# Kernel tuning notes

Measured on AMD Instinct MI355X. Metric: run time of the kernel, lower is better.

The kernel has to match this reference:

```python
import jax, jax.numpy as jnp
import numpy as np

RANK = 16
ALPHA = 16.0
SCALING = ALPHA / RANK
N_ADAPTERS = 8
IN_F = 4096
OUT_F = 4096
BATCH = 4
SEQ = 2048


def setup_inputs() -> dict:
    key = jax.random.key(0)
    kx, ka, kb, ki = jax.random.split(key, 4)
    x = jax.random.normal(kx, (BATCH, SEQ, IN_F), dtype=jnp.float32)
    # A init: randn * 0.02 (as in module). B is zeros in the module; use small
    # random values here so the baseline output/grads are non-trivial.
    A = jax.random.normal(ka, (N_ADAPTERS, OUT_F, RANK), dtype=jnp.float32) * 0.02
    B = jax.random.normal(kb, (N_ADAPTERS, RANK, IN_F), dtype=jnp.float32) * 0.02
    adapter_ids = jax.random.randint(ki, (BATCH,), 0, N_ADAPTERS, dtype=jnp.int32)
    return {"x": x, "A": A, "B": B, "adapter_ids": adapter_ids}


def reference(x, A, B, adapter_ids):
    # Original: Bx = einsum('bni,ari->bnar', x, B); res = einsum('bnar,aor->bnao', Bx, A)
    # then res[arange(b), :, adapter_ids] * scaling.
    # Equivalent (gather-then-batched-GEMM): select each batch element's adapter
    # first, avoiding the O(n_adapters) dense intermediate. Same math.
    B_sel = B[adapter_ids]            # [b, r, in]
    A_sel = A[adapter_ids]            # [b, out, r]
    Bx = jnp.einsum('bni,bri->bnr', x, B_sel)   # [b, n, r]
    out = jnp.einsum('bnr,bor->bno', Bx, A_sel)  # [b, n, out]
    return out * SCALING
```

## Files before the change

### kernel.cpp

```cpp
#include <hip/hip_runtime.h>
#include <hip/hip_bf16.h>

#define RANK   16
#define IN_F   4096
#define OUT_F  4096
#define NBATCH 4
#define SEQLEN 2048
#define NROWS  (NBATCH * SEQLEN)

typedef __bf16 bf16x8   __attribute__((ext_vector_type(8)));
typedef float  floatx4  __attribute__((ext_vector_type(4)));
typedef float  floatx16 __attribute__((ext_vector_type(16)));

static __device__ __forceinline__ bf16x8 load_cvt8(const float* __restrict__ p) {
    floatx4 a = *reinterpret_cast<const floatx4*>(p);
    floatx4 b = *reinterpret_cast<const floatx4*>(p + 4);
    bf16x8 r;
    r[0] = (__bf16)a[0]; r[1] = (__bf16)a[1]; r[2] = (__bf16)a[2]; r[3] = (__bf16)a[3];
    r[4] = (__bf16)b[0]; r[5] = (__bf16)b[1]; r[6] = (__bf16)b[2]; r[7] = (__bf16)b[3];
    return r;
}

__global__ __launch_bounds__(256) void
lora_bx_kernel(const float* __restrict__ x, const float* __restrict__ Bw,
               const int* __restrict__ ids, __bf16* __restrict__ bx)
{
    const int tile = blockIdx.x;
    const int row0 = tile * 16;
    const int adapter = ids[row0 / SEQLEN];
    const int wave = threadIdx.x >> 6;
    const int lane = threadIdx.x & 63;
    const int m    = lane & 15;
    const int quad = lane >> 4;

    const float* xp = x + (size_t)(row0 + m) * IN_F + quad * 8 + wave * 1024;
    const float* bp = Bw + (size_t)adapter * (RANK * IN_F)
                         + (size_t)m * IN_F + quad * 8 + wave * 1024;

    floatx4 acc = {0.f, 0.f, 0.f, 0.f};
#pragma unroll 8
    for (int s = 0; s < 32; ++s) {
        bf16x8 af = load_cvt8(xp + s * 32);
        bf16x8 bf = load_cvt8(bp + s * 32);
        acc = __builtin_amdgcn_mfma_f32_16x16x32_bf16(af, bf, acc, 0, 0, 0);
    }

    __shared__ float red[4][256];
#pragma unroll
    for (int j = 0; j < 4; ++j)
        red[wave][(quad * 4 + j) * 16 + m] = acc[j];
    __syncthreads();

    const int t = threadIdx.x;
    float s = (red[0][t] + red[1][t]) + (red[2][t] + red[3][t]);
    bx[tile * 256 + t] = (__bf16)s;
}

__global__ __launch_bounds__(256) void
lora_out_kernel(const __bf16* __restrict__ bx, const float* __restrict__ Aw,
                const int* __restrict__ ids, float* __restrict__ out)
{
    const int rt    = blockIdx.x >> 2;
    const int chunk = blockIdx.x & 3;
    const int row0  = rt * 32;
    const int adapter = ids[row0 / SEQLEN];
    const int wave = threadIdx.x >> 6;
    const int lane = threadIdx.x & 63;
    const int n    = lane & 31;
    const int half = lane >> 5;

    const bf16x8 a_bx = *reinterpret_cast<const bf16x8*>(
        bx + rt * 512 + n * 16 + half * 8);

    const float* ap = Aw + (size_t)adapter * (OUT_F * RANK) + half * 8;
    const int colbase = chunk * 1024 + wave * 256;

#pragma unroll
    for (int tcol = 0; tcol < 8; ++tcol) {
        const int col0 = colbase + tcol * 32;
        bf16x8 bfrag = load_cvt8(ap + (size_t)(col0 + n) * RANK);
        floatx16 c;
#pragma unroll
        for (int i = 0; i < 16; ++i) c[i] = 0.f;
        c = __builtin_amdgcn_mfma_f32_32x32x16_bf16(a_bx, bfrag, c, 0, 0, 0);
#pragma unroll
        for (int reg = 0; reg < 16; ++reg) {
            const int r = (reg & 3) + 8 * (reg >> 2) + 4 * half;
            out[(size_t)(row0 + r) * OUT_F + col0 + n] = c[reg];
        }
    }
}

extern "C" void kernel_launch(void* const* d_in, const int* in_sizes, int n_in,
                              void* d_out, int out_size, void* d_ws, size_t ws_size,
                              hipStream_t stream) {
    const float* x   = (const float*)d_in[0];
    const float* Aw  = (const float*)d_in[1];
    const float* Bw  = (const float*)d_in[2];
    const int*   ids = (const int*)d_in[3];
    float* out = (float*)d_out;
    __bf16* bx = (__bf16*)d_ws;

    lora_bx_kernel<<<dim3(NROWS / 16), dim3(256), 0, stream>>>(x, Bw, ids, bx);
    lora_out_kernel<<<dim3((NROWS / 32) * 4), dim3(256), 0, stream>>>(bx, Aw, ids, out);
}
```

Baseline: 251.1 us.

## Pre-convert LoRA weights to bf16, split-K the Bx pass, narrow output tiles

Adds a kernel that converts A and B to bf16 once per call, so the GEMM kernels read half-size weights and skip per-load conversion. The Bx kernel is split four ways over K into fp32 partials in workspace, giving four times more blocks. The output kernel sums those partials, works on narrower column chunks with more blocks, and uses nontemporal loads and stores for streamed x and out. The cost is an extra launch, additional workspace traffic for the partials, and reliance on a larger workspace.

```diff
diff --git a/kernel.cpp b/kernel.cpp
--- a/kernel.cpp
+++ b/kernel.cpp
@@ -4,44 +4,60 @@
 #define RANK   16
 #define IN_F   4096
 #define OUT_F  4096
-#define NBATCH 4
 #define SEQLEN 2048
-#define NROWS  (NBATCH * SEQLEN)
+#define NROWS  8192
+#define AB_ELEMS 524288
+#define WSP_QSTRIDE (NROWS * RANK)
 
+typedef __bf16 bf16x4   __attribute__((ext_vector_type(4)));
 typedef __bf16 bf16x8   __attribute__((ext_vector_type(8)));
 typedef float  floatx4  __attribute__((ext_vector_type(4)));
 typedef float  floatx16 __attribute__((ext_vector_type(16)));
 
-static __device__ __forceinline__ bf16x8 load_cvt8(const float* __restrict__ p) {
-    floatx4 a = *reinterpret_cast<const floatx4*>(p);
-    floatx4 b = *reinterpret_cast<const floatx4*>(p + 4);
-    bf16x8 r;
-    r[0] = (__bf16)a[0]; r[1] = (__bf16)a[1]; r[2] = (__bf16)a[2]; r[3] = (__bf16)a[3];
-    r[4] = (__bf16)b[0]; r[5] = (__bf16)b[1]; r[6] = (__bf16)b[2]; r[7] = (__bf16)b[3];
-    return r;
+__global__ __launch_bounds__(256) void
+cvt_ab_kernel(const float* __restrict__ A, const float* __restrict__ Bw,
+              __bf16* __restrict__ A16, __bf16* __restrict__ B16)
+{
+    const int idx = (blockIdx.x * 256 + threadIdx.x) * 4;
+    floatx4 a = *reinterpret_cast<const floatx4*>(A + idx);
+    floatx4 b = *reinterpret_cast<const floatx4*>(Bw + idx);
+    bf16x4 a4, b4;
+#pragma unroll
+    for (int i = 0; i < 4; ++i) { a4[i] = (__bf16)a[i]; b4[i] = (__bf16)b[i]; }
+    *reinterpret_cast<bf16x4*>(A16 + idx) = a4;
+    *reinterpret_cast<bf16x4*>(B16 + idx) = b4;
 }
 
-__global__ __launch_bounds__(256) void
-lora_bx_kernel(const float* __restrict__ x, const float* __restrict__ Bw,
-               const int* __restrict__ ids, __bf16* __restrict__ bx)
+__global__ __launch_bounds__(256, 8) void
+lora_bx_partial(const float* __restrict__ x, const __bf16* __restrict__ B16,
+                const int* __restrict__ ids, float* __restrict__ wsP)
 {
-    const int tile = blockIdx.x;
+    const int tile = blockIdx.x >> 2;
+    const int q    = blockIdx.x & 3;
     const int row0 = tile * 16;
     const int adapter = ids[row0 / SEQLEN];
     const int wave = threadIdx.x >> 6;
     const int lane = threadIdx.x & 63;
     const int m    = lane & 15;
     const int quad = lane >> 4;
+    const int k0   = q * 1024 + wave * 256;
 
-    const float* xp = x + (size_t)(row0 + m) * IN_F + quad * 8 + wave * 1024;
-    const float* bp = Bw + (size_t)adapter * (RANK * IN_F)
-                         + (size_t)m * IN_F + quad * 8 + wave * 1024;
+    const float*  xp = x + (size_t)(row0 + m) * IN_F + k0 + quad * 8;
+    const __bf16* bp = B16 + adapter * (RANK * IN_F) + m * IN_F + k0 + quad * 8;
 
     floatx4 acc = {0.f, 0.f, 0.f, 0.f};
-#pragma unroll 8
-    for (int s = 0; s < 32; ++s) {
-        bf16x8 af = load_cvt8(xp + s * 32);
-        bf16x8 bf = load_cvt8(bp + s * 32);
+#pragma unroll
+    for (int s = 0; s < 8; ++s) {
+        floatx4 xa = __builtin_nontemporal_load(
+            reinterpret_cast<const floatx4*>(xp + s * 32));
+        floatx4 xb = __builtin_nontemporal_load(
+            reinterpret_cast<const floatx4*>(xp + s * 32 + 4));
+        bf16x8 bf = *reinterpret_cast<const bf16x8*>(bp + s * 32);
+        bf16x8 af;
+        af[0] = (__bf16)xa[0]; af[1] = (__bf16)xa[1];
+        af[2] = (__bf16)xa[2]; af[3] = (__bf16)xa[3];
+        af[4] = (__bf16)xb[0]; af[5] = (__bf16)xb[1];
+        af[6] = (__bf16)xb[2]; af[7] = (__bf16)xb[3];
         acc = __builtin_amdgcn_mfma_f32_16x16x32_bf16(af, bf, acc, 0, 0, 0);
     }
 
@@ -53,15 +69,15 @@
 
     const int t = threadIdx.x;
     float s = (red[0][t] + red[1][t]) + (red[2][t] + red[3][t]);
-    bx[tile * 256 + t] = (__bf16)s;
+    wsP[(size_t)q * WSP_QSTRIDE + tile * 256 + t] = s;
 }
 
-__global__ __launch_bounds__(256) void
-lora_out_kernel(const __bf16* __restrict__ bx, const float* __restrict__ Aw,
+__global__ __launch_bounds__(256, 8) void
+lora_out_kernel(const float* __restrict__ wsP, const __bf16* __restrict__ A16,
                 const int* __restrict__ ids, float* __restrict__ out)
 {
-    const int rt    = blockIdx.x >> 2;
-    const int chunk = blockIdx.x & 3;
+    const int rt    = blockIdx.x >> 3;
+    const int chunk = blockIdx.x & 7;
     const int row0  = rt * 32;
     const int adapter = ids[row0 / SEQLEN];
     const int wave = threadIdx.x >> 6;
@@ -69,16 +85,28 @@
     const int n    = lane & 31;
     const int half = lane >> 5;
 
-    const bf16x8 a_bx = *reinterpret_cast<const bf16x8*>(
-        bx + rt * 512 + n * 16 + half * 8);
+    const float* pp = wsP + (size_t)(row0 + n) * RANK + half * 8;
+    floatx4 s0 = *reinterpret_cast<const floatx4*>(pp);
+    floatx4 s1 = *reinterpret_cast<const floatx4*>(pp + 4);
+#pragma unroll
+    for (int q = 1; q < 4; ++q) {
+        s0 += *reinterpret_cast<const floatx4*>(pp + q * WSP_QSTRIDE);
+        s1 += *reinterpret_cast<const floatx4*>(pp + q * WSP_QSTRIDE + 4);
+    }
+    bf16x8 a_bx;
+    a_bx[0] = (__bf16)s0[0]; a_bx[1] = (__bf16)s0[1];
+    a_bx[2] = (__bf16)s0[2]; a_bx[3] = (__bf16)s0[3];
+    a_bx[4] = (__bf16)s1[0]; a_bx[5] = (__bf16)s1[1];
+    a_bx[6] = (__bf16)s1[2]; a_bx[7] = (__bf16)s1[3];
 
-    const float* ap = Aw + (size_t)adapter * (OUT_F * RANK) + half * 8;
-    const int colbase = chunk * 1024 + wave * 256;
+    const __bf16* ap = A16 + adapter * (OUT_F * RANK) + half * 8;
+    const int colbase = chunk * 512 + wave * 128;
 
 #pragma unroll
-    for (int tcol = 0; tcol < 8; ++tcol) {
+    for (int tcol = 0; tcol < 4; ++tcol) {
         const int col0 = colbase + tcol * 32;
-        bf16x8 bfrag = load_cvt8(ap + (size_t)(col0 + n) * RANK);
+        bf16x8 bfrag = *reinterpret_cast<const bf16x8*>(
+            ap + (size_t)(col0 + n) * RANK);
         floatx16 c;
 #pragma unroll
         for (int i = 0; i < 16; ++i) c[i] = 0.f;
@@ -86,7 +114,8 @@
 #pragma unroll
         for (int reg = 0; reg < 16; ++reg) {
             const int r = (reg & 3) + 8 * (reg >> 2) + 4 * half;
-            out[(size_t)(row0 + r) * OUT_F + col0 + n] = c[reg];
+            __builtin_nontemporal_store(
+                c[reg], out + (size_t)(row0 + r) * OUT_F + col0 + n);
         }
     }
 }
@@ -99,8 +128,12 @@
     const float* Bw  = (const float*)d_in[2];
     const int*   ids = (const int*)d_in[3];
     float* out = (float*)d_out;
-    __bf16* bx = (__bf16*)d_ws;
 
-    lora_bx_kernel<<<dim3(NROWS / 16), dim3(256), 0, stream>>>(x, Bw, ids, bx);
-    lora_out_kernel<<<dim3((NROWS / 32) * 4), dim3(256), 0, stream>>>(bx, Aw, ids, out);
+    __bf16* A16 = (__bf16*)d_ws;
+    __bf16* B16 = A16 + AB_ELEMS;
+    float*  wsP = (float*)(B16 + AB_ELEMS);
+
+    cvt_ab_kernel <<<dim3(AB_ELEMS / 1024), dim3(256), 0, stream>>>(Aw, Bw, A16, B16);
+    lora_bx_partial<<<dim3(512 * 4),         dim3(256), 0, stream>>>(x, B16, ids, wsP);
+    lora_out_kernel<<<dim3(256 * 8),         dim3(256), 0, stream>>>(wsP, A16, ids, out);
 }
```

Result: no change. 252.3 us (+0.5%).

## Fuse Bx and output GEMMs into one kernel with shared-memory Bx

Applied to the files above, without the earlier changes.

Merges the two kernels into one 512-thread kernel per 16-row tile. Eight waves split the K reduction for Bx and reduce it in shared memory, then the same block computes all output columns from the bf16 Bx tile. This removes the workspace round-trip and the second launch. Output stores become nontemporal. The 32x32 MFMA wastes half its rows because only the 16 valid rows are stored, and each block now walks the full A matrix.

```diff
diff --git a/kernel.cpp b/kernel.cpp
--- a/kernel.cpp
+++ b/kernel.cpp
@@ -4,89 +4,87 @@
 #define RANK   16
 #define IN_F   4096
 #define OUT_F  4096
-#define NBATCH 4
 #define SEQLEN 2048
-#define NROWS  (NBATCH * SEQLEN)
+#define NROWS  8192
 
 typedef __bf16 bf16x8   __attribute__((ext_vector_type(8)));
 typedef float  floatx4  __attribute__((ext_vector_type(4)));
 typedef float  floatx16 __attribute__((ext_vector_type(16)));
 
-static __device__ __forceinline__ bf16x8 load_cvt8(const float* __restrict__ p) {
-    floatx4 a = *reinterpret_cast<const floatx4*>(p);
-    floatx4 b = *reinterpret_cast<const floatx4*>(p + 4);
+static __device__ __forceinline__ bf16x8 cvt8(floatx4 a, floatx4 b) {
     bf16x8 r;
     r[0] = (__bf16)a[0]; r[1] = (__bf16)a[1]; r[2] = (__bf16)a[2]; r[3] = (__bf16)a[3];
     r[4] = (__bf16)b[0]; r[5] = (__bf16)b[1]; r[6] = (__bf16)b[2]; r[7] = (__bf16)b[3];
     return r;
 }
 
-__global__ __launch_bounds__(256) void
-lora_bx_kernel(const float* __restrict__ x, const float* __restrict__ Bw,
-               const int* __restrict__ ids, __bf16* __restrict__ bx)
+__global__ __launch_bounds__(512, 4) void
+lora_fused_kernel(const float* __restrict__ x, const float* __restrict__ Aw,
+                  const float* __restrict__ Bw, const int* __restrict__ ids,
+                  float* __restrict__ out)
 {
     const int tile = blockIdx.x;
     const int row0 = tile * 16;
-    const int adapter = ids[row0 / SEQLEN];
-    const int wave = threadIdx.x >> 6;
-    const int lane = threadIdx.x & 63;
-    const int m    = lane & 15;
-    const int quad = lane >> 4;
+    const int adapter = ids[row0 >> 11];
+    const int tid  = threadIdx.x;
+    const int wave = tid >> 6;
+    const int lane = tid & 63;
 
-    const float* xp = x + (size_t)(row0 + m) * IN_F + quad * 8 + wave * 1024;
-    const float* bp = Bw + (size_t)adapter * (RANK * IN_F)
-                         + (size_t)m * IN_F + quad * 8 + wave * 1024;
+    __shared__ float  red[8][256];
+    __shared__ __bf16 bxs[256];
 
-    floatx4 acc = {0.f, 0.f, 0.f, 0.f};
-#pragma unroll 8
-    for (int s = 0; s < 32; ++s) {
-        bf16x8 af = load_cvt8(xp + s * 32);
-        bf16x8 bf = load_cvt8(bp + s * 32);
-        acc = __builtin_amdgcn_mfma_f32_16x16x32_bf16(af, bf, acc, 0, 0, 0);
+    {
+        const int m    = lane & 15;
+        const int quad = lane >> 4;
+        const int k0   = wave * 512 + quad * 8;
+        const float* xp = x + (size_t)(row0 + m) * IN_F + k0;
+        const float* bp = Bw + (size_t)adapter * (RANK * IN_F) + m * IN_F + k0;
+
+        floatx4 acc = {0.f, 0.f, 0.f, 0.f};
+#pragma unroll
+        for (int s = 0; s < 16; ++s) {
+            floatx4 xa = *reinterpret_cast<const floatx4*>(xp + s * 32);
+            floatx4 xb = *reinterpret_cast<const floatx4*>(xp + s * 32 + 4);
+            floatx4 ba = *reinterpret_cast<const floatx4*>(bp + s * 32);
+            floatx4 bb = *reinterpret_cast<const floatx4*>(bp + s * 32 + 4);
+            acc = __builtin_amdgcn_mfma_f32_16x16x32_bf16(
+                cvt8(xa, xb), cvt8(ba, bb), acc, 0, 0, 0);
+        }
+#pragma unroll
+        for (int j = 0; j < 4; ++j)
+            red[wave][(quad * 4 + j) * 16 + m] = acc[j];
     }
-
-    __shared__ float red[4][256];
-#pragma unroll
-    for (int j = 0; j < 4; ++j)
-        red[wave][(quad * 4 + j) * 16 + m] = acc[j];
+    __syncthreads();
+    if (tid < 256) {
+        float s = ((red[0][tid] + red[1][tid]) + (red[2][tid] + red[3][tid]))
+                + ((red[4][tid] + red[5][tid]) + (red[6][tid] + red[7][tid]));
+        bxs[tid] = (__bf16)s;
+    }
     __syncthreads();
 
-    const int t = threadIdx.x;
-    float s = (red[0][t] + red[1][t]) + (red[2][t] + red[3][t]);
-    bx[tile * 256 + t] = (__bf16)s;
-}
+    {
+        const int n    = lane & 31;
+        const int half = lane >> 5;
+        const int mm   = n & 15;
 
-__global__ __launch_bounds__(256) void
-lora_out_kernel(const __bf16* __restrict__ bx, const float* __restrict__ Aw,
-                const int* __restrict__ ids, float* __restrict__ out)
-{
-    const int rt    = blockIdx.x >> 2;
-    const int chunk = blockIdx.x & 3;
-    const int row0  = rt * 32;
-    const int adapter = ids[row0 / SEQLEN];
-    const int wave = threadIdx.x >> 6;
-    const int lane = threadIdx.x & 63;
-    const int n    = lane & 31;
-    const int half = lane >> 5;
+        const bf16x8 a_bx = *reinterpret_cast<const bf16x8*>(bxs + mm * 16 + half * 8);
+        const float* ap = Aw + (size_t)adapter * (OUT_F * RANK) + half * 8;
 
-    const bf16x8 a_bx = *reinterpret_cast<const bf16x8*>(
-        bx + rt * 512 + n * 16 + half * 8);
-
-    const float* ap = Aw + (size_t)adapter * (OUT_F * RANK) + half * 8;
-    const int colbase = chunk * 1024 + wave * 256;
-
+#pragma unroll 4
+        for (int t = 0; t < 16; ++t) {
+            const int col0 = (wave * 16 + t) * 32;
+            floatx4 fa = *reinterpret_cast<const floatx4*>(ap + (size_t)(col0 + n) * RANK);
+            floatx4 fb = *reinterpret_cast<const floatx4*>(ap + (size_t)(col0 + n) * RANK + 4);
+            floatx16 c;
 #pragma unroll
-    for (int tcol = 0; tcol < 8; ++tcol) {
-        const int col0 = colbase + tcol * 32;
-        bf16x8 bfrag = load_cvt8(ap + (size_t)(col0 + n) * RANK);
-        floatx16 c;
+            for (int i = 0; i < 16; ++i) c[i] = 0.f;
+            c = __builtin_amdgcn_mfma_f32_32x32x16_bf16(a_bx, cvt8(fa, fb), c, 0, 0, 0);
 #pragma unroll
-        for (int i = 0; i < 16; ++i) c[i] = 0.f;
-        c = __builtin_amdgcn_mfma_f32_32x32x16_bf16(a_bx, bfrag, c, 0, 0, 0);
-#pragma unroll
-        for (int reg = 0; reg < 16; ++reg) {
-            const int r = (reg & 3) + 8 * (reg >> 2) + 4 * half;
-            out[(size_t)(row0 + r) * OUT_F + col0 + n] = c[reg];
+            for (int reg = 0; reg < 8; ++reg) {
+                const int r = (reg & 3) + 8 * (reg >> 2) + 4 * half;
+                __builtin_nontemporal_store(
+                    c[reg], out + (size_t)(row0 + r) * OUT_F + col0 + n);
+            }
         }
     }
 }
@@ -99,8 +97,6 @@
     const float* Bw  = (const float*)d_in[2];
     const int*   ids = (const int*)d_in[3];
     float* out = (float*)d_out;
-    __bf16* bx = (__bf16*)d_ws;
 
-    lora_bx_kernel<<<dim3(NROWS / 16), dim3(256), 0, stream>>>(x, Bw, ids, bx);
-    lora_out_kernel<<<dim3((NROWS / 32) * 4), dim3(256), 0, stream>>>(bx, Aw, ids, out);
+    lora_fused_kernel<<<dim3(NROWS / 16), dim3(512), 0, stream>>>(x, Aw, Bw, ids, out);
 }
```

Measured after the change: 250.5 us. About the same (-0.2%).
